# Kernel optimization log

Measured on AMD Instinct MI355X. Metric: run time of the kernel, lower is better.

Reference implementation:

```python
import jax, jax.numpy as jnp
import numpy as np

WS = 8          # window size
HEAD_DIM = 32
C = 128
B, H, W = 8, 256, 256


def _grid_sample(img, grid):
    # torch F.grid_sample, bilinear, padding_mode='zeros', align_corners=True
    # img [N,C,Hi,Wi]; grid [N,Ho,Wo,2] with (x,y) in [-1,1]
    N, Cc, Hi, Wi = img.shape
    gx = (grid[..., 0] + 1.0) * 0.5 * (Wi - 1)
    gy = (grid[..., 1] + 1.0) * 0.5 * (Hi - 1)
    x0 = jnp.floor(gx); y0 = jnp.floor(gy)
    wx1 = gx - x0; wy1 = gy - y0

    def gather(ix, iy):
        valid = ((ix >= 0) & (ix < Wi) & (iy >= 0) & (iy < Hi)).astype(img.dtype)
        ixc = jnp.clip(ix, 0, Wi - 1).astype(jnp.int32)
        iyc = jnp.clip(iy, 0, Hi - 1).astype(jnp.int32)
        v = jax.vmap(lambda im, yy, xx: im[:, yy, xx])(img, iyc, ixc)  # [N,C,Ho,Wo]
        return v * valid[:, None]

    return (gather(x0, y0) * ((1 - wx1) * (1 - wy1))[:, None]
            + gather(x0 + 1, y0) * (wx1 * (1 - wy1))[:, None]
            + gather(x0, y0 + 1) * ((1 - wx1) * wy1)[:, None]
            + gather(x0 + 1, y0 + 1) * (wx1 * wy1)[:, None])


def _rel_bias(rpp):
    cord = np.array([[i, j] for i in range(WS) for j in range(WS)])
    rel = cord[:, None, :] - cord[None, :, :] + WS - 1   # [p2,p2,2]
    return rpp[:, rel[..., 0], rel[..., 1]]               # [h,p2,p2]


def _mask(w1, w2, p, shift):
    s = p - shift
    m = np.zeros((w1, w2, p, p, p, p), dtype=bool)
    m[-1, :, :s, :, s:, :] = True
    m[-1, :, s:, :, :s, :] = True
    m[:, -1, :, :s, :, s:] = True
    m[:, -1, :, s:, :, :s] = True
    return jnp.asarray(m.reshape(1, 1, w1 * w2, p * p, p * p))


def setup_inputs() -> dict:
    key = jax.random.key(0)
    ks = jax.random.split(key, 8)
    s = 0.02
    return {
        'x': jax.random.normal(ks[0], (B, H, W, C), jnp.float32),
        'rpp': jax.random.normal(ks[1], (C // HEAD_DIM, 2 * WS - 1, 2 * WS - 1), jnp.float32) * s,
        'wi_w': jax.random.normal(ks[2], (C, 2), jnp.float32) * s,
        'wi_b': jnp.zeros((2,), jnp.float32),
        'w1_w': jax.random.normal(ks[3], (C, 2), jnp.float32) * s,
        'w1_b': jnp.zeros((2,), jnp.float32),
        'w2_w': jax.random.normal(ks[4], (WS * WS * 2, 2), jnp.float32) * s,
        'w2_b': jnp.zeros((2,), jnp.float32),
        'q_w': jax.random.normal(ks[5], (C, C), jnp.float32) * s,
        'q_b': jnp.zeros((C,), jnp.float32),
        'kv_w': jax.random.normal(ks[6], (C, 2 * C), jnp.float32) * s,
        'kv_b': jnp.zeros((2 * C,), jnp.float32),
        'o_w': jax.random.normal(ks[7], (C, C), jnp.float32) * s,
        'o_b': jnp.zeros((C,), jnp.float32),
    }


def reference(x, rpp, wi_w, wi_b, w1_w, w1_b, w2_w, w2_b, q_w, q_b, kv_w, kv_b, o_w, o_b):
    shift = WS // 2
    b, Hh, Ww, c = x.shape
    w1, w2 = Hh // WS, Ww // WS
    nw, p2 = w1 * w2, WS * WS
    h = c // HEAD_DIM

    # cyclic shift (type != 'W')
    x = jnp.roll(x, (-shift, -shift), axis=(1, 2))
    xw = x.reshape(b, w1, WS, w2, WS, c).transpose(0, 1, 3, 2, 4, 5)  # [b,w1,w2,p,p,c]

    off_intra = xw @ wi_w + wi_b                                       # [b,w1,w2,p,p,2]
    oi = xw @ w1_w + w1_b                                              # [b,w1,w2,p,p,2]
    oi = oi.reshape(b, w1, w2, WS * WS * 2) @ w2_w + w2_b              # [b,w1,w2,2]

    # --- inter-window deformable sampling ---
    gy, gx = np.meshgrid(np.arange(w1), np.arange(w2), indexing='ij')
    gridw = jnp.asarray(np.stack((gx, gy), -1), jnp.float32)           # [w1,w2,2]
    og = gridw[None, :, :, None, None, :] + oi[:, :, :, None, None, :]
    og = jnp.broadcast_to(og, (b, w1, w2, WS, WS, 2))
    og = og / ((max(w1, w2) - 1) / 2) - 1.0
    ximg = xw.transpose(0, 3, 4, 5, 1, 2).reshape(b * p2, c, w1, w2)
    gint = og.transpose(0, 3, 4, 1, 2, 5).reshape(b * p2, w1, w2, 2)
    xd = _grid_sample(ximg, gint)                                      # [b*p2,c,w1,w2]
    xd = xd.reshape(b, WS, WS, c, w1, w2).transpose(0, 4, 5, 1, 2, 3)  # [b,w1,w2,p,p,c]

    # --- intra-window deformable sampling ---
    gy, gx = np.meshgrid(np.arange(WS), np.arange(WS), indexing='ij')
    gridp = jnp.asarray(np.stack((gx, gy), -1), jnp.float32)           # [p,p,2]
    og2 = gridp[None, None] + off_intra.reshape(b, nw, WS, WS, 2)
    og2 = og2 / ((WS - 1) / 2) - 1.0
    xd2 = xd.transpose(0, 1, 2, 5, 3, 4).reshape(b * nw, c, WS, WS)
    g2 = og2.reshape(b * nw, WS, WS, 2)
    xd2 = _grid_sample(xd2, g2).reshape(b, w1, w2, c, WS, WS).transpose(0, 1, 2, 4, 5, 3)

    # --- windowed attention ---
    xq = xw.reshape(b, nw, p2, c)
    xkv = xd2.reshape(b, nw, p2, c)
    q = (xq @ q_w + q_b).reshape(b, nw, p2, h, HEAD_DIM).transpose(3, 0, 1, 2, 4)
    kv = (xkv @ kv_w + kv_b).reshape(b, nw, p2, 2 * h, HEAD_DIM)
    k = kv[..., :h, :].transpose(3, 0, 1, 2, 4)
    v = kv[..., h:, :].transpose(3, 0, 1, 2, 4)

    scale = HEAD_DIM ** (-0.5)
    sim = jnp.einsum('hbwpc,hbwqc->hbwpq', q, k) * scale
    sim = sim + _rel_bias(rpp)[:, None, None]
    sim = jnp.where(_mask(w1, w2, WS, shift), -jnp.inf, sim)
    probs = jax.nn.softmax(sim, axis=-1)
    out = jnp.einsum('hbwpq,hbwqc->hbwpc', probs, v)
    out = out.transpose(1, 2, 3, 0, 4).reshape(b, nw, p2, c)
    out = out @ o_w + o_b
    out = out.reshape(b, w1, w2, WS, WS, c).transpose(0, 1, 3, 2, 4, 5).reshape(b, Hh, Ww, c)
    out = jnp.roll(out, (shift, shift), axis=(1, 2))
    return out
```

## Files before the change

kernel.cpp:

```cpp
#include <hip/hip_runtime.h>
#include <hip/hip_bf16.h>


#define WS_    8
#define SHIFT_ 4
#define C_     128
#define IMG_   256

typedef __attribute__((ext_vector_type(8))) short short8;
typedef __attribute__((ext_vector_type(4))) short short4v;
typedef __attribute__((ext_vector_type(4))) float f32x4;

#define MFMA(a,b,c) __builtin_amdgcn_mfma_f32_16x16x32_bf16((a),(b),(c),0,0,0)

__device__ __forceinline__ short f2bf(float f){
    unsigned u = __float_as_uint(f);
    u = u + 0x7fffu + ((u >> 16) & 1u);
    return (short)(u >> 16);
}
__device__ __forceinline__ float bf2f(short s){
    return __uint_as_float(((unsigned)(unsigned short)s) << 16);
}

__global__ void dgwa_prep(const float* __restrict__ q_w, const float* __restrict__ kv_w,
                          const float* __restrict__ o_w, short* __restrict__ ws){
    int idx = blockIdx.x*256 + threadIdx.x;
    if (idx < 16384){ int co = idx>>7, ci = idx&127; ws[idx] = f2bf(q_w[ci*128 + co]); }
    else if (idx < 49152){ int i = idx-16384; int co = i>>7, ci = i&127; ws[idx] = f2bf(kv_w[ci*256 + co]); }
    else { int i = idx-49152; int co = i>>7, ci = i&127; ws[idx] = f2bf(o_w[ci*128 + co]); }
}

__global__ __launch_bounds__(512, 2)
void dgwa_fused(const float* __restrict__ x, const float* __restrict__ rpp,
                const float* __restrict__ wi_w, const float* __restrict__ wi_b,
                const float* __restrict__ w1_w, const float* __restrict__ w1_b,
                const float* __restrict__ w2_w, const float* __restrict__ w2_b,
                const float* __restrict__ q_b,  const float* __restrict__ kv_b,
                const float* __restrict__ o_b,
                const short* __restrict__ wsw,
                float* __restrict__ out)
{
    __shared__ __align__(16) char smem[147992];
    short* s_w    = (short*)(smem);
    short* s_xd   = (short*)(smem);
    short* s_p    = (short*)(smem + 34816);
    short* s_xw   = (short*)(smem + 72704);
    short* s_xd2  = (short*)(smem + 90112);
    float* s_outT = (float*)(smem + 90112);
    short* s_k    = (short*)(smem + 107520);
    short* s_vT   = (short*)(smem + 124928);
    float* s_rpp  = (float*)(smem + 143360);
    float* s_off  = (float*)(smem + 146960);
    float* s_red  = (float*)(smem + 147472);
    float* s_oi   = (float*)(smem + 147984);

    const int t   = threadIdx.x;
    const int wv  = t >> 6, l = t & 63, l15 = l & 15, quad = l >> 4;
    const int win = blockIdx.x;
    const int bb  = win >> 10, wy = (win >> 5) & 31, wx = win & 31;
    const f32x4 zf = {0.f, 0.f, 0.f, 0.f};

    {
        const int tok = t >> 3, part = t & 7;
        const int i = tok >> 3, j = tok & 7;
        const int grow = (wy*8 + i + SHIFT_) & 255;
        const int gcol = (wx*8 + j + SHIFT_) & 255;
        const float* xr = x + (((size_t)bb*IMG_ + grow)*IMG_ + gcol)*C_ + part*16;
        float di0=0.f, di1=0.f, d10=0.f, d11=0.f;
        #pragma unroll
        for (int c4 = 0; c4 < 4; ++c4){
            const float4 a4 = *(const float4*)(xr + c4*4);
            const int ch = part*16 + c4*4;
            di0 += a4.x*wi_w[ch*2+0]+a4.y*wi_w[ch*2+2]+a4.z*wi_w[ch*2+4]+a4.w*wi_w[ch*2+6];
            di1 += a4.x*wi_w[ch*2+1]+a4.y*wi_w[ch*2+3]+a4.z*wi_w[ch*2+5]+a4.w*wi_w[ch*2+7];
            d10 += a4.x*w1_w[ch*2+0]+a4.y*w1_w[ch*2+2]+a4.z*w1_w[ch*2+4]+a4.w*w1_w[ch*2+6];
            d11 += a4.x*w1_w[ch*2+1]+a4.y*w1_w[ch*2+3]+a4.z*w1_w[ch*2+5]+a4.w*w1_w[ch*2+7];
            short4v sv = { f2bf(a4.x), f2bf(a4.y), f2bf(a4.z), f2bf(a4.w) };
            *(short4v*)&s_xw[tok*136 + part*16 + c4*4] = sv;
        }
        di0 += __shfl_xor(di0,1); di0 += __shfl_xor(di0,2); di0 += __shfl_xor(di0,4);
        di1 += __shfl_xor(di1,1); di1 += __shfl_xor(di1,2); di1 += __shfl_xor(di1,4);
        d10 += __shfl_xor(d10,1); d10 += __shfl_xor(d10,2); d10 += __shfl_xor(d10,4);
        d11 += __shfl_xor(d11,1); d11 += __shfl_xor(d11,2); d11 += __shfl_xor(d11,4);
        if (part == 0){
            s_off[tok*2+0] = di0 + wi_b[0];
            s_off[tok*2+1] = di1 + wi_b[1];
            s_red[tok*2+0] = d10 + w1_b[0];
            s_red[tok*2+1] = d11 + w1_b[1];
        }
    }
    for (int idx = t; idx < 900; idx += 512) s_rpp[idx] = rpp[idx];
    __syncthreads();
    if (t < 64){
        const float a0 = s_red[t*2+0], a1 = s_red[t*2+1];
        float p0 = a0*w2_w[(t*2+0)*2+0] + a1*w2_w[(t*2+1)*2+0];
        float p1 = a0*w2_w[(t*2+0)*2+1] + a1*w2_w[(t*2+1)*2+1];
        #pragma unroll
        for (int m = 1; m < 64; m <<= 1){ p0 += __shfl_xor(p0,m); p1 += __shfl_xor(p1,m); }
        if (t == 0){ s_oi[0] = p0 + w2_b[0]; s_oi[1] = p1 + w2_b[1]; }
    }
    __syncthreads();

    {
        const int tok = t >> 3, part = t & 7;
        const int i = tok >> 3, j = tok & 7;
        const float gx = (float)wx + s_oi[0];
        const float gy = (float)wy + s_oi[1];
        const float fx0 = floorf(gx), fy0 = floorf(gy);
        const int ix0 = (int)fx0, iy0 = (int)fy0;
        const float fx = gx - fx0, fy = gy - fy0;
        const float cw[4] = {(1.f-fx)*(1.f-fy), fx*(1.f-fy), (1.f-fx)*fy, fx*fy};
        float4 acc4[4];
        #pragma unroll
        for (int c4 = 0; c4 < 4; ++c4) acc4[c4] = make_float4(0.f,0.f,0.f,0.f);
        #pragma unroll
        for (int cc = 0; cc < 4; ++cc){
            const int cx = ix0 + (cc & 1), cy = iy0 + (cc >> 1);
            if (cx >= 0 && cx < 32 && cy >= 0 && cy < 32){
                const int rr = (cy*8 + i + SHIFT_) & 255;
                const int cl = (cx*8 + j + SHIFT_) & 255;
                const float* p = x + (((size_t)bb*IMG_ + rr)*IMG_ + cl)*C_ + part*16;
                const float w = cw[cc];
                #pragma unroll
                for (int c4 = 0; c4 < 4; ++c4){
                    const float4 v = *(const float4*)(p + c4*4);
                    acc4[c4].x += w*v.x; acc4[c4].y += w*v.y;
                    acc4[c4].z += w*v.z; acc4[c4].w += w*v.w;
                }
            }
        }
        #pragma unroll
        for (int c4 = 0; c4 < 4; ++c4){
            short4v sv = { f2bf(acc4[c4].x), f2bf(acc4[c4].y), f2bf(acc4[c4].z), f2bf(acc4[c4].w) };
            *(short4v*)&s_xd[tok*136 + part*16 + c4*4] = sv;
        }
    }
    __syncthreads();

    {
        const int tok = t >> 3, part = t & 7;
        const int i = tok >> 3, j = tok & 7;
        const float sx = (float)j + s_off[tok*2+0];
        const float sy = (float)i + s_off[tok*2+1];
        const float fx0 = floorf(sx), fy0 = floorf(sy);
        const int jx0 = (int)fx0, jy0 = (int)fy0;
        const float fx = sx - fx0, fy = sy - fy0;
        float4 acc4[4];
        #pragma unroll
        for (int c4 = 0; c4 < 4; ++c4) acc4[c4] = make_float4(0.f,0.f,0.f,0.f);
        #pragma unroll
        for (int cc = 0; cc < 4; ++cc){
            const int cx = jx0 + (cc & 1), cy = jy0 + (cc >> 1);
            const float w = ((cc & 1) ? fx : 1.f-fx) * ((cc >> 1) ? fy : 1.f-fy);
            if (cx >= 0 && cx < 8 && cy >= 0 && cy < 8){
                const short* p = &s_xd[(cy*8 + cx)*136 + part*16];
                #pragma unroll
                for (int c4 = 0; c4 < 4; ++c4){
                    const short4v sv = *(const short4v*)(p + c4*4);
                    acc4[c4].x += w*bf2f(sv.x); acc4[c4].y += w*bf2f(sv.y);
                    acc4[c4].z += w*bf2f(sv.z); acc4[c4].w += w*bf2f(sv.w);
                }
            }
        }
        #pragma unroll
        for (int c4 = 0; c4 < 4; ++c4){
            short4v sv = { f2bf(acc4[c4].x), f2bf(acc4[c4].y), f2bf(acc4[c4].z), f2bf(acc4[c4].w) };
            *(short4v*)&s_xd2[tok*136 + part*16 + c4*4] = sv;
        }
    }
    __syncthreads();

    {
        const short* src = wsw + 16384;
        #pragma unroll
        for (int r8 = 0; r8 < 8; ++r8){
            const int e = (r8*512 + t)*8;
            *(short8*)&s_w[(e>>7)*136 + (e&127)] = *(const short8*)&src[e];
        }
    }
    __syncthreads();
    {
        f32x4 acc[2][4];
        #pragma unroll
        for (int nn = 0; nn < 2; ++nn)
            #pragma unroll
            for (int mt = 0; mt < 4; ++mt) acc[nn][mt] = zf;
        #pragma unroll
        for (int ks = 0; ks < 4; ++ks){
            const int co = ks*32 + quad*8;
            const short8 b0 = *(const short8*)&s_w[(32*wv +      l15)*136 + co];
            const short8 b1 = *(const short8*)&s_w[(32*wv + 16 + l15)*136 + co];
            #pragma unroll
            for (int mt = 0; mt < 4; ++mt){
                const short8 a = *(const short8*)&s_xd2[(16*mt + l15)*136 + co];
                acc[0][mt] = MFMA(a, b0, acc[0][mt]);
                acc[1][mt] = MFMA(a, b1, acc[1][mt]);
            }
        }
        #pragma unroll
        for (int nn = 0; nn < 2; ++nn){
            const int col = 32*wv + 16*nn + l15;
            const float bias = kv_b[col];
            #pragma unroll
            for (int mt = 0; mt < 4; ++mt){
                #pragma unroll
                for (int r = 0; r < 4; ++r){
                    const int tokr = 16*mt + 4*quad + r;
                    const short v = f2bf(acc[nn][mt][r] + bias);
                    if (col < 128) s_k[tokr*136 + col] = v;
                    else           s_vT[(col-128)*72 + tokr] = v;
                }
            }
        }
    }
    __syncthreads();

    {
        #pragma unroll
        for (int r4 = 0; r4 < 4; ++r4){
            const int e = (r4*512 + t)*8;
            *(short8*)&s_w[(e>>7)*136 + (e&127)] = *(const short8*)&wsw[e];
        }
    }
    __syncthreads();
    {
        f32x4 qacc[4];
        #pragma unroll
        for (int mt = 0; mt < 4; ++mt) qacc[mt] = zf;
        #pragma unroll
        for (int ks = 0; ks < 4; ++ks){
            const int co = ks*32 + quad*8;
            const short8 b = *(const short8*)&s_w[(16*wv + l15)*136 + co];
            #pragma unroll
            for (int mt = 0; mt < 4; ++mt){
                const short8 a = *(const short8*)&s_xw[(16*mt + l15)*136 + co];
                qacc[mt] = MFMA(a, b, qacc[mt]);
            }
        }
        __syncthreads();
        const int col = 16*wv + l15;
        const float bias = q_b[col];
        #pragma unroll
        for (int mt = 0; mt < 4; ++mt)
            #pragma unroll
            for (int r = 0; r < 4; ++r)
                s_xw[(16*mt + 4*quad + r)*136 + col] = f2bf(qacc[mt][r] + bias);
    }
    __syncthreads();

    if (wv < 4){
        const int h = wv;
        short8 a[4], bq[4];
        #pragma unroll
        for (int mt = 0; mt < 4; ++mt)
            a[mt]  = *(const short8*)&s_k [(16*mt + l15)*136 + 32*h + quad*8];
        #pragma unroll
        for (int nt = 0; nt < 4; ++nt)
            bq[nt] = *(const short8*)&s_xw[(16*nt + l15)*136 + 32*h + quad*8];
        f32x4 sc[4][4];
        #pragma unroll
        for (int mt = 0; mt < 4; ++mt)
            #pragma unroll
            for (int nt = 0; nt < 4; ++nt)
                sc[mt][nt] = MFMA(a[mt], bq[nt], zf);
        const bool mrow = (wy == 31), mcol = (wx == 31);
        float rs[4];
        #pragma unroll
        for (int nt = 0; nt < 4; ++nt){
            const int qtok = 16*nt + l15;
            const int iq = qtok >> 3, jq = qtok & 7;
            float ssum = 0.f;
            #pragma unroll
            for (int mt = 0; mt < 4; ++mt){
                #pragma unroll
                for (int r = 0; r < 4; ++r){
                    const int ktok = 16*mt + 4*quad + r;
                    const int ik = ktok >> 3, jk = ktok & 7;
                    const float sv = sc[mt][nt][r]*0.1767766952966369f
                                   + s_rpp[h*225 + (iq-ik+7)*15 + (jq-jk+7)];
                    const bool masked = (mrow && ((iq<4)!=(ik<4))) || (mcol && ((jq<4)!=(jk<4)));
                    const float e = masked ? 0.f : __expf(sv);
                    sc[mt][nt][r] = e;
                    ssum += e;
                }
            }
            ssum += __shfl_xor(ssum, 16);
            ssum += __shfl_xor(ssum, 32);
            rs[nt] = 1.f / ssum;
        }
        #pragma unroll
        for (int nt = 0; nt < 4; ++nt){
            const int qtok = 16*nt + l15;
            #pragma unroll
            for (int mt = 0; mt < 4; ++mt)
                #pragma unroll
                for (int r = 0; r < 4; ++r){
                    const int ktok = 16*mt + 4*quad + r;
                    s_p[h*4608 + qtok*72 + ktok] = f2bf(sc[mt][nt][r] * rs[nt]);
                }
        }
    } else {
        const int tt = t - 256;
        const short* src = wsw + 49152;
        #pragma unroll
        for (int r8 = 0; r8 < 8; ++r8){
            const int e = (r8*256 + tt)*8;
            *(short8*)&s_w[(e>>7)*136 + (e&127)] = *(const short8*)&src[e];
        }
    }
    __syncthreads();

    {
        const int h = wv >> 1, mh = wv & 1;
        short8 av[2];
        #pragma unroll
        for (int ks = 0; ks < 2; ++ks)
            av[ks] = *(const short8*)&s_vT[(32*h + 16*mh + l15)*72 + ks*32 + quad*8];
        f32x4 po[4];
        #pragma unroll
        for (int nt = 0; nt < 4; ++nt) po[nt] = zf;
        #pragma unroll
        for (int nt = 0; nt < 4; ++nt)
            #pragma unroll
            for (int ks = 0; ks < 2; ++ks){
                const short8 bp = *(const short8*)&s_p[h*4608 + (16*nt + l15)*72 + ks*32 + quad*8];
                po[nt] = MFMA(av[ks], bp, po[nt]);
            }
        #pragma unroll
        for (int nt = 0; nt < 4; ++nt){
            const int qtok = 16*nt + l15;
            #pragma unroll
            for (int r = 0; r < 4; ++r){
                const int drow = 32*h + 16*mh + 4*quad + r;
                s_xw[qtok*136 + drow] = f2bf(po[nt][r]);
            }
        }
    }
    __syncthreads();

    {
        f32x4 oc[4];
        #pragma unroll
        for (int nt = 0; nt < 4; ++nt) oc[nt] = zf;
        #pragma unroll
        for (int ks = 0; ks < 4; ++ks){
            const int co = ks*32 + quad*8;
            const short8 aw = *(const short8*)&s_w[(16*wv + l15)*136 + co];
            #pragma unroll
            for (int nt = 0; nt < 4; ++nt){
                const short8 bt = *(const short8*)&s_xw[(16*nt + l15)*136 + co];
                oc[nt] = MFMA(aw, bt, oc[nt]);
            }
        }
        const float4 ob = *(const float4*)&o_b[16*wv + 4*quad];
        const float obr[4] = {ob.x, ob.y, ob.z, ob.w};
        #pragma unroll
        for (int nt = 0; nt < 4; ++nt){
            const int tok = 16*nt + l15;
            #pragma unroll
            for (int r = 0; r < 4; ++r){
                const int cout = 16*wv + 4*quad + r;
                s_outT[cout*65 + tok] = oc[nt][r] + obr[r];
            }
        }
    }
    __syncthreads();

    {
        const int chan = t & 127;
        #pragma unroll
        for (int it = 0; it < 16; ++it){
            const int tok = (t >> 7) + it*4;
            const int i = tok >> 3, j = tok & 7;
            const int orow = (wy*8 + i + SHIFT_) & 255;
            const int ocol = (wx*8 + j + SHIFT_) & 255;
            out[(((size_t)bb*IMG_ + orow)*IMG_ + ocol)*C_ + chan] = s_outT[chan*65 + tok];
        }
    }
}

extern "C" void kernel_launch(void* const* d_in, const int* in_sizes, int n_in,
                              void* d_out, int out_size, void* d_ws, size_t ws_size,
                              hipStream_t stream) {
    (void)in_sizes; (void)n_in; (void)out_size; (void)ws_size;
    const float* x    = (const float*)d_in[0];
    const float* rpp  = (const float*)d_in[1];
    const float* wi_w = (const float*)d_in[2];
    const float* wi_b = (const float*)d_in[3];
    const float* w1_w = (const float*)d_in[4];
    const float* w1_b = (const float*)d_in[5];
    const float* w2_w = (const float*)d_in[6];
    const float* w2_b = (const float*)d_in[7];
    const float* q_w  = (const float*)d_in[8];
    const float* q_b  = (const float*)d_in[9];
    const float* kv_w = (const float*)d_in[10];
    const float* kv_b = (const float*)d_in[11];
    const float* o_w  = (const float*)d_in[12];
    const float* o_b  = (const float*)d_in[13];
    float* out = (float*)d_out;
    short* ws  = (short*)d_ws;

    dgwa_prep<<<dim3(256), dim3(256), 0, stream>>>(q_w, kv_w, o_w, ws);
    dgwa_fused<<<dim3(8192), dim3(512), 0, stream>>>(
        x, rpp, wi_w, wi_b, w1_w, w1_b, w2_w, w2_b,
        q_b, kv_b, o_b, ws, out);
}
```

Measured before the change: 913.6 us.

## Shrink LDS footprint by reading weights from global and aliasing buffers

Stops staging the q/kv/o weight matrices in shared memory and has MFMA operands read directly from global (L2-cached) bf16 weights. It re-aliases the LDS buffers so per-block shared memory drops to about half, and raises the launch-bounds occupancy target from 2 to 4 blocks. It also packs bf16 stores into 32-bit writes, restructures the softmax to compute scores per query tile, and adjusts strides (68, 66) to reduce bank conflicts. The trade-off is extra global-memory loads of weights per block and tighter register limits.

```diff
diff --git a/kernel.cpp b/kernel.cpp
--- a/kernel.cpp
+++ b/kernel.cpp
@@ -30,7 +30,7 @@
     else { int i = idx-49152; int co = i>>7, ci = i&127; ws[idx] = f2bf(o_w[ci*128 + co]); }
 }
 
-__global__ __launch_bounds__(512, 2)
+__global__ __launch_bounds__(512, 4)
 void dgwa_fused(const float* __restrict__ x, const float* __restrict__ rpp,
                 const float* __restrict__ wi_w, const float* __restrict__ wi_b,
                 const float* __restrict__ w1_w, const float* __restrict__ w1_b,
@@ -40,25 +40,28 @@
                 const short* __restrict__ wsw,
                 float* __restrict__ out)
 {
-    __shared__ __align__(16) char smem[147992];
-    short* s_w    = (short*)(smem);
-    short* s_xd   = (short*)(smem);
-    short* s_p    = (short*)(smem + 34816);
-    short* s_xw   = (short*)(smem + 72704);
-    short* s_xd2  = (short*)(smem + 90112);
-    float* s_outT = (float*)(smem + 90112);
-    short* s_k    = (short*)(smem + 107520);
-    short* s_vT   = (short*)(smem + 124928);
-    float* s_rpp  = (float*)(smem + 143360);
-    float* s_off  = (float*)(smem + 146960);
-    float* s_red  = (float*)(smem + 147472);
-    float* s_oi   = (float*)(smem + 147984);
+    __shared__ __align__(16) char smem[75296];
+    short* s_xw   = (short*)(smem);
+    short* s_xd2  = (short*)(smem + 17408);
+    short* s_p    = (short*)(smem + 17408);
+    float* s_outT = (float*)(smem + 17408);
+    short* s_k    = (short*)(smem + 34816);
+    short* s_xd   = (short*)(smem + 34816);
+    short* s_vT   = (short*)(smem + 52224);
+    float* s_rpp  = (float*)(smem + 70656);
+    float* s_off  = (float*)(smem + 74256);
+    float* s_red  = (float*)(smem + 74768);
+    float* s_oi   = (float*)(smem + 75280);
 
     const int t   = threadIdx.x;
     const int wv  = t >> 6, l = t & 63, l15 = l & 15, quad = l >> 4;
     const int win = blockIdx.x;
     const int bb  = win >> 10, wy = (win >> 5) & 31, wx = win & 31;
     const f32x4 zf = {0.f, 0.f, 0.f, 0.f};
+
+    const short* qw  = wsw;
+    const short* kvw = wsw + 16384;
+    const short* ow  = wsw + 49152;
 
     {
         const int tok = t >> 3, part = t & 7;
@@ -171,15 +174,6 @@
     __syncthreads();
 
     {
-        const short* src = wsw + 16384;
-        #pragma unroll
-        for (int r8 = 0; r8 < 8; ++r8){
-            const int e = (r8*512 + t)*8;
-            *(short8*)&s_w[(e>>7)*136 + (e&127)] = *(const short8*)&src[e];
-        }
-    }
-    __syncthreads();
-    {
         f32x4 acc[2][4];
         #pragma unroll
         for (int nn = 0; nn < 2; ++nn)
@@ -188,8 +182,8 @@
         #pragma unroll
         for (int ks = 0; ks < 4; ++ks){
             const int co = ks*32 + quad*8;
-            const short8 b0 = *(const short8*)&s_w[(32*wv +      l15)*136 + co];
-            const short8 b1 = *(const short8*)&s_w[(32*wv + 16 + l15)*136 + co];
+            const short8 b0 = *(const short8*)&kvw[(32*wv +      l15)*128 + co];
+            const short8 b1 = *(const short8*)&kvw[(32*wv + 16 + l15)*128 + co];
             #pragma unroll
             for (int mt = 0; mt < 4; ++mt){
                 const short8 a = *(const short8*)&s_xd2[(16*mt + l15)*136 + co];
@@ -201,28 +195,30 @@
         for (int nn = 0; nn < 2; ++nn){
             const int col = 32*wv + 16*nn + l15;
             const float bias = kv_b[col];
-            #pragma unroll
-            for (int mt = 0; mt < 4; ++mt){
-                #pragma unroll
-                for (int r = 0; r < 4; ++r){
-                    const int tokr = 16*mt + 4*quad + r;
-                    const short v = f2bf(acc[nn][mt][r] + bias);
-                    if (col < 128) s_k[tokr*136 + col] = v;
-                    else           s_vT[(col-128)*72 + tokr] = v;
-                }
-            }
-        }
-    }
-    __syncthreads();
-
-    {
-        #pragma unroll
-        for (int r4 = 0; r4 < 4; ++r4){
-            const int e = (r4*512 + t)*8;
-            *(short8*)&s_w[(e>>7)*136 + (e&127)] = *(const short8*)&wsw[e];
-        }
-    }
-    __syncthreads();
+            if (col < 128){
+                #pragma unroll
+                for (int mt = 0; mt < 4; ++mt)
+                    #pragma unroll
+                    for (int r = 0; r < 4; ++r){
+                        const int tokr = 16*mt + 4*quad + r;
+                        s_k[tokr*136 + col] = f2bf(acc[nn][mt][r] + bias);
+                    }
+            } else {
+                const int vr = col - 128;
+                #pragma unroll
+                for (int mt = 0; mt < 4; ++mt)
+                    #pragma unroll
+                    for (int rp = 0; rp < 2; ++rp){
+                        const int tokr = 16*mt + 4*quad + 2*rp;
+                        const unsigned lo = (unsigned short)f2bf(acc[nn][mt][2*rp]   + bias);
+                        const unsigned hi = (unsigned short)f2bf(acc[nn][mt][2*rp+1] + bias);
+                        *(unsigned*)&s_vT[vr*72 + tokr] = lo | (hi << 16);
+                    }
+            }
+        }
+    }
+    __syncthreads();
+
     {
         f32x4 qacc[4];
         #pragma unroll
@@ -230,7 +226,7 @@
         #pragma unroll
         for (int ks = 0; ks < 4; ++ks){
             const int co = ks*32 + quad*8;
-            const short8 b = *(const short8*)&s_w[(16*wv + l15)*136 + co];
+            const short8 b = *(const short8*)&qw[(16*wv + l15)*128 + co];
             #pragma unroll
             for (int mt = 0; mt < 4; ++mt){
                 const short8 a = *(const short8*)&s_xw[(16*mt + l15)*136 + co];
@@ -248,25 +244,26 @@
     }
     __syncthreads();
 
+    short8 ka[4], bq[4];
     if (wv < 4){
         const int h = wv;
-        short8 a[4], bq[4];
         #pragma unroll
         for (int mt = 0; mt < 4; ++mt)
-            a[mt]  = *(const short8*)&s_k [(16*mt + l15)*136 + 32*h + quad*8];
+            ka[mt] = *(const short8*)&s_k [(16*mt + l15)*136 + 32*h + quad*8];
         #pragma unroll
         for (int nt = 0; nt < 4; ++nt)
             bq[nt] = *(const short8*)&s_xw[(16*nt + l15)*136 + 32*h + quad*8];
-        f32x4 sc[4][4];
-        #pragma unroll
-        for (int mt = 0; mt < 4; ++mt)
-            #pragma unroll
-            for (int nt = 0; nt < 4; ++nt)
-                sc[mt][nt] = MFMA(a[mt], bq[nt], zf);
+    }
+    __syncthreads();
+    if (wv < 4){
+        const int h = wv;
         const bool mrow = (wy == 31), mcol = (wx == 31);
-        float rs[4];
         #pragma unroll
         for (int nt = 0; nt < 4; ++nt){
+            f32x4 sc[4];
+            #pragma unroll
+            for (int mt = 0; mt < 4; ++mt)
+                sc[mt] = MFMA(ka[mt], bq[nt], zf);
             const int qtok = 16*nt + l15;
             const int iq = qtok >> 3, jq = qtok & 7;
             float ssum = 0.f;
@@ -276,36 +273,26 @@
                 for (int r = 0; r < 4; ++r){
                     const int ktok = 16*mt + 4*quad + r;
                     const int ik = ktok >> 3, jk = ktok & 7;
-                    const float sv = sc[mt][nt][r]*0.1767766952966369f
+                    const float sv = sc[mt][r]*0.1767766952966369f
                                    + s_rpp[h*225 + (iq-ik+7)*15 + (jq-jk+7)];
                     const bool masked = (mrow && ((iq<4)!=(ik<4))) || (mcol && ((jq<4)!=(jk<4)));
                     const float e = masked ? 0.f : __expf(sv);
-                    sc[mt][nt][r] = e;
+                    sc[mt][r] = e;
                     ssum += e;
                 }
             }
             ssum += __shfl_xor(ssum, 16);
             ssum += __shfl_xor(ssum, 32);
-            rs[nt] = 1.f / ssum;
-        }
-        #pragma unroll
-        for (int nt = 0; nt < 4; ++nt){
-            const int qtok = 16*nt + l15;
+            const float rs = 1.f / ssum;
             #pragma unroll
             for (int mt = 0; mt < 4; ++mt)
                 #pragma unroll
-                for (int r = 0; r < 4; ++r){
-                    const int ktok = 16*mt + 4*quad + r;
-                    s_p[h*4608 + qtok*72 + ktok] = f2bf(sc[mt][nt][r] * rs[nt]);
+                for (int rp = 0; rp < 2; ++rp){
+                    const int ktok = 16*mt + 4*quad + 2*rp;
+                    const unsigned lo = (unsigned short)f2bf(sc[mt][2*rp]   * rs);
+                    const unsigned hi = (unsigned short)f2bf(sc[mt][2*rp+1] * rs);
+                    *(unsigned*)&s_p[h*4352 + qtok*68 + ktok] = lo | (hi << 16);
                 }
-        }
-    } else {
-        const int tt = t - 256;
-        const short* src = wsw + 49152;
-        #pragma unroll
-        for (int r8 = 0; r8 < 8; ++r8){
-            const int e = (r8*256 + tt)*8;
-            *(short8*)&s_w[(e>>7)*136 + (e&127)] = *(const short8*)&src[e];
         }
     }
     __syncthreads();
@@ -323,16 +310,18 @@
         for (int nt = 0; nt < 4; ++nt)
             #pragma unroll
             for (int ks = 0; ks < 2; ++ks){
-                const short8 bp = *(const short8*)&s_p[h*4608 + (16*nt + l15)*72 + ks*32 + quad*8];
+                const short8 bp = *(const short8*)&s_p[h*4352 + (16*nt + l15)*68 + ks*32 + quad*8];
                 po[nt] = MFMA(av[ks], bp, po[nt]);
             }
         #pragma unroll
         for (int nt = 0; nt < 4; ++nt){
             const int qtok = 16*nt + l15;
             #pragma unroll
-            for (int r = 0; r < 4; ++r){
-                const int drow = 32*h + 16*mh + 4*quad + r;
-                s_xw[qtok*136 + drow] = f2bf(po[nt][r]);
+            for (int rp = 0; rp < 2; ++rp){
+                const int drow = 32*h + 16*mh + 4*quad + 2*rp;
+                const unsigned lo = (unsigned short)f2bf(po[nt][2*rp]);
+                const unsigned hi = (unsigned short)f2bf(po[nt][2*rp+1]);
+                *(unsigned*)&s_xw[qtok*136 + drow] = lo | (hi << 16);
             }
         }
     }
@@ -345,7 +334,7 @@
         #pragma unroll
         for (int ks = 0; ks < 4; ++ks){
             const int co = ks*32 + quad*8;
-            const short8 aw = *(const short8*)&s_w[(16*wv + l15)*136 + co];
+            const short8 aw = *(const short8*)&ow[(16*wv + l15)*128 + co];
             #pragma unroll
             for (int nt = 0; nt < 4; ++nt){
                 const short8 bt = *(const short8*)&s_xw[(16*nt + l15)*136 + co];
@@ -360,7 +349,7 @@
             #pragma unroll
             for (int r = 0; r < 4; ++r){
                 const int cout = 16*wv + 4*quad + r;
-                s_outT[cout*65 + tok] = oc[nt][r] + obr[r];
+                s_outT[cout*66 + tok] = oc[nt][r] + obr[r];
             }
         }
     }
@@ -374,7 +363,7 @@
             const int i = tok >> 3, j = tok & 7;
             const int orow = (wy*8 + i + SHIFT_) & 255;
             const int ocol = (wx*8 + j + SHIFT_) & 255;
-            out[(((size_t)bb*IMG_ + orow)*IMG_ + ocol)*C_ + chan] = s_outT[chan*65 + tok];
+            out[(((size_t)bb*IMG_ + orow)*IMG_ + ocol)*C_ + chan] = s_outT[chan*66 + tok];
         }
     }
 }
```

New measurement: 765.8 us. -16.2%, faster.
